# Kernel tuning notes

Hardware: AMD Instinct MI355X
Metric: run time of the kernel (lower is better)

The kernel has to match this reference:

```python
import jax, jax.numpy as jnp
import numpy as np

BETA_MAX = 0.995
BETA_MIN = 0.05
EPI_AGE_PENALTY = 0.02
EPI_STRENGTH_BOOST = 0.5
EPI_STRENGTH_DECAY = 0.995
EPI_WRITE_ALPHA = 0.5
EVICT_AGE_BOOST = 0.05
EVICT_STR_PENALTY = 0.5
SLOT_TEMP = 50.0
SWITCH_TAU = 0.5

B, H, K, U, OBS, SSUM, PROJ = 2048, 256, 32, 128, 128, 128, 128


def setup_inputs() -> dict:
    key = jax.random.key(0)
    ks = jax.random.split(key, 20)
    def gl(k, shape, fan_in):
        return jax.random.normal(k, shape, jnp.float32) / np.sqrt(fan_in).astype(np.float32)
    inp = {}
    inp['h_prev'] = jax.random.normal(ks[0], (B, H), jnp.float32)
    inp['keys'] = jax.random.normal(ks[1], (B, K, H), jnp.float32)
    inp['vals'] = jax.random.normal(ks[2], (B, K, H), jnp.float32)
    inp['age'] = jax.random.uniform(ks[3], (B, K), jnp.float32) * 100.0
    inp['strength'] = jax.random.uniform(ks[4], (B, K), jnp.float32)
    inp['obs'] = jax.random.normal(ks[5], (B, OBS), jnp.float32)
    inp['ssum'] = jax.random.normal(ks[6], (B, SSUM), jnp.float32)
    inp['u_int_prev'] = jax.random.normal(ks[7], (B, U), jnp.float32)
    inp['step_in_macro'] = jax.random.randint(ks[8], (B,), 0, 4, jnp.int32)
    # learned parameters
    inp['W_obs'] = gl(ks[9], (OBS, PROJ), OBS); inp['b_obs'] = jnp.zeros((PROJ,), jnp.float32)
    inp['W_ssum'] = gl(ks[10], (SSUM, PROJ), SSUM); inp['b_ssum'] = jnp.zeros((PROJ,), jnp.float32)
    XIN = 2 * PROJ
    inp['Wi'] = gl(ks[11], (XIN, 3 * H), XIN); inp['bi'] = jnp.zeros((3 * H,), jnp.float32)
    inp['Wh'] = gl(ks[12], (H, 3 * H), H); inp['bhn'] = jnp.zeros((H,), jnp.float32)
    inp['W_gate'] = gl(ks[13], (H, 1), H); inp['b_gate'] = jnp.zeros((1,), jnp.float32)
    inp['W_mean'] = gl(ks[14], (2 * H, U), 2 * H); inp['b_mean'] = jnp.zeros((U,), jnp.float32)
    inp['u_logstd'] = jnp.full((U,), -1.0, jnp.float32)
    inp['W_beta'] = gl(ks[15], (2 * H, 1), 2 * H); inp['b_beta'] = jnp.zeros((1,), jnp.float32)
    inp['W_sw'] = gl(ks[16], (2 * H, 1), 2 * H); inp['b_sw'] = jnp.zeros((1,), jnp.float32)
    return inp


def reference(h_prev, keys, vals, age, strength, obs, ssum, u_int_prev, step_in_macro,
              W_obs, b_obs, W_ssum, b_ssum, Wi, bi, Wh, bhn, W_gate, b_gate,
              W_mean, b_mean, u_logstd, W_beta, b_beta, W_sw, b_sw):
    Kslots = keys.shape[1]
    # input projections + GRU step (flax GRUCell: h' = (1-z)*n + z*h)
    xo = jnp.tanh(obs @ W_obs + b_obs)
    xs = jnp.tanh(ssum @ W_ssum + b_ssum)
    x_in = jnp.concatenate([xo, xs], axis=-1)
    gi = x_in @ Wi + bi
    gh = h_prev @ Wh
    ir, iz, inn = jnp.split(gi, 3, axis=-1)
    hr, hz, hn = jnp.split(gh, 3, axis=-1)
    r = jax.nn.sigmoid(ir + hr)
    z = jax.nn.sigmoid(iz + hz)
    n = jnp.tanh(inn + r * (hn + bhn))
    h_t = (1.0 - z) * n + z * h_prev
    # write gate
    w_str = jax.nn.sigmoid(h_t @ W_gate + b_gate)  # [B,1]
    # episodic slot memory: cosine-sim read
    qn = h_t / (jnp.linalg.norm(h_t, axis=-1, keepdims=True) + 1e-6)
    kn = keys / (jnp.linalg.norm(keys, axis=-1, keepdims=True) + 1e-6)
    sim_r = jnp.einsum('bkd,bd->bk', kn, qn)
    logits = sim_r + EPI_STRENGTH_BOOST * jnp.log(jnp.clip(strength, 1e-3, 1.0)) - EPI_AGE_PENALTY * age
    w_read = jax.nn.softmax(logits, axis=-1)
    read_out = jnp.einsum('bk,bkd->bd', w_read, vals)
    # write addressing (write_vec == query_vec == h_t so sim_w == sim_r)
    wk_n = qn
    sim_w = sim_r
    evict = EVICT_AGE_BOOST * jnp.log1p(age) - EVICT_STR_PENALTY * strength
    write_soft = jax.nn.softmax(sim_w * SLOT_TEMP + evict, axis=-1)
    write_hard = jax.nn.one_hot(jnp.argmax(write_soft, axis=-1), Kslots, dtype=jnp.float32)
    write_w = jax.lax.stop_gradient(write_hard - write_soft) + write_soft  # straight-through
    ws = jnp.clip(w_str, 0.0, 1.0)  # [B,1]
    eff_rate = write_w * ws * EPI_WRITE_ALPHA  # [B,K]
    rate = eff_rate[:, :, None]
    keys_new = (1.0 - rate) * keys + rate * wk_n[:, None, :]
    vals_new = (1.0 - rate) * vals + rate * h_t[:, None, :]
    age_new = (age + 1.0) * (1.0 - write_w)
    str_new = strength * EPI_STRENGTH_DECAY
    str_new = jnp.clip(str_new + write_w * ws * (1.0 - str_new), 0.0, 1.0)
    # heads
    ctx = jnp.concatenate([h_t, read_out], axis=-1)
    mean = ctx @ W_mean + b_mean
    beta = BETA_MIN + (BETA_MAX - BETA_MIN) * jax.nn.sigmoid((ctx @ W_beta + b_beta)[:, 0])
    sw_prob = jax.nn.sigmoid((ctx @ W_sw + b_sw)[:, 0])
    # deterministic path (rng=None): u_prop = mean, threshold switch
    u_prop = mean
    switch_f = jnp.where(sw_prob > SWITCH_TAU, 1.0, 0.0)
    is_boundary = jnp.where(step_in_macro == 0, 1.0, 0.0)
    switch_f = jnp.maximum(switch_f, is_boundary)
    sw_f = switch_f[:, None]
    beta_eff = beta[:, None] * (1.0 - sw_f)
    u_int = beta_eff * u_int_prev + (1.0 - beta_eff) * u_prop
    return (h_t, keys_new, vals_new, age_new, str_new, u_prop,
            switch_f.astype(jnp.int32), u_int, beta, sw_prob)
```

## Files before the change

### kernel.cpp

```cpp
#include <hip/hip_runtime.h>
#include <math.h>

#define Bdim 2048
#define Hdim 256
#define KS 32
#define Udim 128
#define OBSD 128
#define PROJD 128
#define H3 768

__device__ __forceinline__ float sigm(float x){ return 1.0f/(1.0f+__expf(-x)); }

typedef float __attribute__((ext_vector_type(4))) f32x4;

__device__ __forceinline__ float4 ntload4(const float* p){
    f32x4 v = __builtin_nontemporal_load((const f32x4*)p);
    return make_float4(v.x, v.y, v.z, v.w);
}

__global__ __launch_bounds__(256) void kA1(
    const float* __restrict__ obs, const float* __restrict__ ssum,
    const float* __restrict__ W_obs, const float* __restrict__ b_obs,
    const float* __restrict__ W_ssum, const float* __restrict__ b_ssum,
    float* __restrict__ xin)
{
    __shared__ float s_in[2][8][128];
    const int t = threadIdx.x;
    const int r0 = blockIdx.x * 8;

    {
        int r = t >> 5, c4 = (t & 31) << 2;
        float4 v = *(const float4*)(obs + (size_t)(r0+r)*OBSD + c4);
        s_in[0][r][c4+0]=v.x; s_in[0][r][c4+1]=v.y; s_in[0][r][c4+2]=v.z; s_in[0][r][c4+3]=v.w;
        v = *(const float4*)(ssum + (size_t)(r0+r)*OBSD + c4);
        s_in[1][r][c4+0]=v.x; s_in[1][r][c4+1]=v.y; s_in[1][r][c4+2]=v.z; s_in[1][r][c4+3]=v.w;
    }
    __syncthreads();

    const int col = t & 127;
    const int src = t >> 7;
    const float* Wp = src ? W_ssum : W_obs;
    const float bb = src ? b_ssum[col] : b_obs[col];

    float acc[8] = {0,0,0,0,0,0,0,0};
    for (int i=0;i<128;i++){
        float w = Wp[i*PROJD + col];
        #pragma unroll
        for (int r=0;r<8;r++) acc[r] = fmaf(s_in[src][r][i], w, acc[r]);
    }
    #pragma unroll
    for (int r=0;r<8;r++)
        xin[(size_t)(r0+r)*256 + t] = tanhf(acc[r] + bb);
}

__global__ __launch_bounds__(256) void kG2(
    const float* __restrict__ xin, const float* __restrict__ hp,
    const float* __restrict__ Wi, const float* __restrict__ Wh,
    float* __restrict__ g)
{
    __shared__ float Xt[2][16][68];
    __shared__ float Wt[2][16][64];

    const int t = threadIdx.x;
    const int bx = blockIdx.x >> 4;
    const int by = blockIdx.x & 15;
    const int r0 = bx * 64;
    const int c0 = by * 64;

    const int kbeg = (c0 >= 768) ? 256 : 0;
    const int kend = (c0 >= 512 && c0 < 768) ? 256 : 512;
    const int nck  = (kend - kbeg) >> 4;

    const int sr  = t >> 2;
    const int sk4 = (t & 3) << 2;
    const size_t xbase = (size_t)(r0 + sr) * 256 + sk4;
    const int wk  = t >> 4;
    const int wc4 = (t & 15) << 2;
    const int cW  = (c0 < 512) ? c0 : (c0 - 256);

    const int rowA = (t & 15) << 2;
    const int colA = (t >> 4) << 2;

    float acc[4][4] = {{0.f}};
    float4 xr, wr;

    {
        const int k0 = kbeg;
        const float* xs = (k0 < 256) ? (xin + xbase + k0) : (hp + xbase + (k0 - 256));
        xr = *(const float4*)xs;
        const int k = k0 + wk;
        const float* wsrc = (k < 256) ? (Wi + (size_t)k*H3 + c0 + wc4)
                                      : (Wh + (size_t)(k-256)*H3 + cW + wc4);
        wr = *(const float4*)wsrc;
    }
    Xt[0][sk4+0][sr] = xr.x; Xt[0][sk4+1][sr] = xr.y;
    Xt[0][sk4+2][sr] = xr.z; Xt[0][sk4+3][sr] = xr.w;
    *(float4*)&Wt[0][wk][wc4] = wr;
    __syncthreads();

    for (int ck = 0; ck < nck; ck++){
        const int cur = ck & 1;
        const bool more = (ck + 1 < nck);
        if (more){
            const int k0 = kbeg + ((ck + 1) << 4);
            const float* xs = (k0 < 256) ? (xin + xbase + k0) : (hp + xbase + (k0 - 256));
            xr = *(const float4*)xs;
            const int k = k0 + wk;
            const float* wsrc = (k < 256) ? (Wi + (size_t)k*H3 + c0 + wc4)
                                          : (Wh + (size_t)(k-256)*H3 + cW + wc4);
            wr = *(const float4*)wsrc;
        }
        #pragma unroll
        for (int kk = 0; kk < 16; kk++){
            float4 a4 = *(const float4*)&Xt[cur][kk][rowA];
            float4 b4 = *(const float4*)&Wt[cur][kk][colA];
            float av[4] = {a4.x, a4.y, a4.z, a4.w};
            float bv[4] = {b4.x, b4.y, b4.z, b4.w};
            #pragma unroll
            for (int i=0;i<4;i++)
                #pragma unroll
                for (int j=0;j<4;j++)
                    acc[i][j] = fmaf(av[i], bv[j], acc[i][j]);
        }
        if (more){
            const int nxt = cur ^ 1;
            Xt[nxt][sk4+0][sr] = xr.x; Xt[nxt][sk4+1][sr] = xr.y;
            Xt[nxt][sk4+2][sr] = xr.z; Xt[nxt][sk4+3][sr] = xr.w;
            *(float4*)&Wt[nxt][wk][wc4] = wr;
            __syncthreads();
        }
    }

    #pragma unroll
    for (int i=0;i<4;i++){
        float4 o = make_float4(acc[i][0], acc[i][1], acc[i][2], acc[i][3]);
        *(float4*)&g[(size_t)(r0 + rowA + i)*1024 + c0 + colA] = o;
    }
}

__global__ __launch_bounds__(256) void kA3(
    const float* __restrict__ g, const float* __restrict__ h_prev,
    const float* __restrict__ bi, const float* __restrict__ bhn,
    const float* __restrict__ W_gate, const float* __restrict__ b_gate,
    const float* __restrict__ W_beta, const float* __restrict__ W_sw,
    const float* __restrict__ W_mean,
    float* __restrict__ out_h, float* __restrict__ ws_invn, float* __restrict__ ws_wstr,
    float* __restrict__ ws_bh, float* __restrict__ ws_sh, float* __restrict__ ws_meanh)
{
    __shared__ float s_h[4][256];
    __shared__ float redA[4][4], redB[4][4], redC[4][4], redD[4][4];
    const int t = threadIdx.x;
    const int r0 = blockIdx.x * 4;

    const float bir = bi[t], biz = bi[t+256], bin_ = bi[t+512];
    const float bh = bhn[t];
    const float wg = W_gate[t];
    const float wb = W_beta[t];
    const float wsw = W_sw[t];
    const int lane = t & 63, wid = t >> 6;

    float hv[4];
    #pragma unroll
    for (int r=0;r<4;r++){
        const size_t gb = (size_t)(r0+r)*1024;
        float gr = g[gb + t];
        float gz = g[gb + 256 + t];
        float gni = g[gb + 512 + t];
        float gnh = g[gb + 768 + t];
        float hp = h_prev[(size_t)(r0+r)*Hdim + t];
        float rr = sigm(gr + bir);
        float zz = sigm(gz + biz);
        float nn = tanhf(gni + bin_ + rr*(gnh + bh));
        hv[r] = (1.0f - zz)*nn + zz*hp;
        s_h[r][t] = hv[r];
    }

    #pragma unroll
    for (int r=0;r<4;r++){
        float a = hv[r]*hv[r];
        float b2 = hv[r]*wg;
        float c2 = hv[r]*wb;
        float d2 = hv[r]*wsw;
        #pragma unroll
        for (int off=32; off>=1; off>>=1){
            a  += __shfl_down(a, off);
            b2 += __shfl_down(b2, off);
            c2 += __shfl_down(c2, off);
            d2 += __shfl_down(d2, off);
        }
        if (lane==0){ redA[r][wid]=a; redB[r][wid]=b2; redC[r][wid]=c2; redD[r][wid]=d2; }
    }
    __syncthreads();
    if (t < 4){
        float ss = redA[t][0]+redA[t][1]+redA[t][2]+redA[t][3];
        float gd = redB[t][0]+redB[t][1]+redB[t][2]+redB[t][3];
        float cb = redC[t][0]+redC[t][1]+redC[t][2]+redC[t][3];
        float cs = redD[t][0]+redD[t][1]+redD[t][2]+redD[t][3];
        ws_invn[r0+t] = 1.0f/(sqrtf(ss) + 1e-6f);
        ws_wstr[r0+t] = sigm(gd + b_gate[0]);
        ws_bh[r0+t] = cb;
        ws_sh[r0+t] = cs;
    }
    #pragma unroll
    for (int r=0;r<4;r++)
        out_h[(size_t)(r0+r)*Hdim + t] = hv[r];
    __syncthreads();

    {
        const int c4 = (t & 31) << 2;
        const int row = (t >> 6);
        const int kh  = (t >> 5) & 1;
        float acc[4] = {0,0,0,0};
        const float* Wm = W_mean + (size_t)kh*128*Udim + c4;
        const float* hr = s_h[row] + kh*128;
        #pragma unroll 8
        for (int i=0;i<128;i++){
            float4 w4 = *(const float4*)(Wm + (size_t)i*Udim);
            float x = hr[i];
            acc[0] = fmaf(x, w4.x, acc[0]);
            acc[1] = fmaf(x, w4.y, acc[1]);
            acc[2] = fmaf(x, w4.z, acc[2]);
            acc[3] = fmaf(x, w4.w, acc[3]);
        }
        __syncthreads();
        s_h[row][kh*128 + c4 + 0] = acc[0];
        s_h[row][kh*128 + c4 + 1] = acc[1];
        s_h[row][kh*128 + c4 + 2] = acc[2];
        s_h[row][kh*128 + c4 + 3] = acc[3];
        __syncthreads();
        const int row2 = t >> 6;
        const int c2 = (t & 63) << 1;
        #pragma unroll
        for (int j=0;j<2;j++){
            int c = c2 + j;
            ws_meanh[(size_t)(r0+row2)*Udim + c] = s_h[row2][c] + s_h[row2][128 + c];
        }
    }
}

__global__ __launch_bounds__(256) void kBC(
    const float* __restrict__ keys, const float* __restrict__ vals,
    const float* __restrict__ age, const float* __restrict__ strength,
    const float* __restrict__ h_t,
    const float* __restrict__ ws_invn, const float* __restrict__ ws_wstr,
    const float* __restrict__ ws_bh, const float* __restrict__ ws_sh,
    const float* __restrict__ ws_meanh,
    const float* __restrict__ u_int_prev, const int* __restrict__ step_in_macro,
    const float* __restrict__ W_mean, const float* __restrict__ b_mean,
    const float* __restrict__ W_beta, const float* __restrict__ b_beta,
    const float* __restrict__ W_sw, const float* __restrict__ b_sw,
    float* __restrict__ keys_new, float* __restrict__ vals_new,
    float* __restrict__ age_new, float* __restrict__ str_new,
    float* __restrict__ out_uprop, float* __restrict__ out_switch,
    float* __restrict__ out_uint, float* __restrict__ out_beta, float* __restrict__ out_swp)
{
    __shared__ float s_sim[KS], s_wr[KS], s_rate[KS];
    __shared__ float4 s_ro[4][64];
    __shared__ float s_rov[256];
    __shared__ float s_part[2][128];
    __shared__ float s_red[2][4];
    __shared__ float s_beff;

    const int b = blockIdx.x;
    const int t = threadIdx.x, lane = t & 63, wid = t >> 6;

    float ag = 0.f, st = 0.f, wstr = 0.f;
    if (t < KS){
        ag = age[b*KS+t];
        st = strength[b*KS+t];
        wstr = ws_wstr[b];
    }

    const float invn = ws_invn[b];
    const float4 h4 = ((const float4*)(h_t + (size_t)b*Hdim))[lane];
    const float4 q4 = make_float4(h4.x*invn, h4.y*invn, h4.z*invn, h4.w*invn);

    const float* Kb = keys + (size_t)b*KS*Hdim;
    const float* Vb = vals + (size_t)b*KS*Hdim;
    float4 kreg[8], vreg[8];
    float v[16];
    #pragma unroll
    for (int s=0;s<8;s++){
        const int k = wid*8 + s;
        kreg[s] = ntload4(Kb + k*Hdim + lane*4);
        vreg[s] = ntload4(Vb + k*Hdim + lane*4);
        v[2*s]   = kreg[s].x*q4.x + kreg[s].y*q4.y + kreg[s].z*q4.z + kreg[s].w*q4.w;
        v[2*s+1] = kreg[s].x*kreg[s].x + kreg[s].y*kreg[s].y + kreg[s].z*kreg[s].z + kreg[s].w*kreg[s].w;
    }

    {
        const bool hb5 = (lane & 32) != 0;
        #pragma unroll
        for (int i=0;i<8;i++){
            float send = hb5 ? v[i] : v[i+8];
            float recv = __shfl_xor(send, 32);
            v[i] = (hb5 ? v[i+8] : v[i]) + recv;
        }
        const bool hb4 = (lane & 16) != 0;
        #pragma unroll
        for (int i=0;i<4;i++){
            float send = hb4 ? v[i] : v[i+4];
            float recv = __shfl_xor(send, 16);
            v[i] = (hb4 ? v[i+4] : v[i]) + recv;
        }
        const bool hb3 = (lane & 8) != 0;
        #pragma unroll
        for (int i=0;i<2;i++){
            float send = hb3 ? v[i] : v[i+2];
            float recv = __shfl_xor(send, 8);
            v[i] = (hb3 ? v[i+2] : v[i]) + recv;
        }
        const bool hb2 = (lane & 4) != 0;
        {
            float send = hb2 ? v[0] : v[1];
            float recv = __shfl_xor(send, 4);
            v[0] = (hb2 ? v[1] : v[0]) + recv;
        }
        float r0 = v[0];
        r0 += __shfl_xor(r0, 2);
        r0 += __shfl_xor(r0, 1);
        float other = __shfl_xor(r0, 4);
        if ((lane & 7) == 0){
            s_sim[wid*8 + (lane>>3)] = r0 / (sqrtf(other) + 1e-6f);
        }
    }
    __syncthreads();

    if (t < KS){
        float sim = s_sim[t];
        float cl = fminf(fmaxf(st, 0.001f), 1.0f);
        float logit = sim + 0.5f*logf(cl) - 0.02f*ag;
        float wl = 50.0f*sim + 0.05f*log1pf(ag) - 0.5f*st;

        float lmax = logit;
        #pragma unroll
        for (int off=16; off>=1; off>>=1)
            lmax = fmaxf(lmax, __shfl_xor(lmax, off));
        float e = __expf(logit - lmax);
        float es = e;
        #pragma unroll
        for (int off=16; off>=1; off>>=1)
            es += __shfl_xor(es, off);

        float wm = wl; int ki = t;
        #pragma unroll
        for (int off=16; off>=1; off>>=1){
            float ow = __shfl_xor(wm, off);
            int   ok = __shfl_xor(ki, off);
            if (ow > wm || (ow == wm && ok < ki)){ wm = ow; ki = ok; }
        }

        s_wr[t] = e / es;
        float hard = (t == ki) ? 1.0f : 0.0f;
        s_rate[t] = hard * 0.5f * wstr;
        age_new[b*KS+t] = (ag + 1.0f)*(1.0f - hard);
        float sd = st*0.995f;
        float sn = sd + hard*wstr*(1.0f - sd);
        str_new[b*KS+t] = fminf(fmaxf(sn,0.f),1.f);
    }
    __syncthreads();

    float4 ro = make_float4(0.f,0.f,0.f,0.f);
    float* KNb = keys_new + (size_t)b*KS*Hdim;
    float* VNb = vals_new + (size_t)b*KS*Hdim;
    #pragma unroll
    for (int s=0;s<8;s++){
        const int k = wid*8 + s;
        const float wr = s_wr[k];
        const float rate = s_rate[k];
        const float om = 1.0f - rate;
        ro.x = fmaf(wr, vreg[s].x, ro.x);
        ro.y = fmaf(wr, vreg[s].y, ro.y);
        ro.z = fmaf(wr, vreg[s].z, ro.z);
        ro.w = fmaf(wr, vreg[s].w, ro.w);
        float4 kn, vn;
        kn.x = om*kreg[s].x + rate*q4.x;
        kn.y = om*kreg[s].y + rate*q4.y;
        kn.z = om*kreg[s].z + rate*q4.z;
        kn.w = om*kreg[s].w + rate*q4.w;
        vn.x = om*vreg[s].x + rate*h4.x;
        vn.y = om*vreg[s].y + rate*h4.y;
        vn.z = om*vreg[s].z + rate*h4.z;
        vn.w = om*vreg[s].w + rate*h4.w;
        *(float4*)(KNb + k*Hdim + lane*4) = kn;
        *(float4*)(VNb + k*Hdim + lane*4) = vn;
    }
    s_ro[wid][lane] = ro;
    __syncthreads();
    if (t < 64){
        float4 a = s_ro[0][t], bb = s_ro[1][t], c = s_ro[2][t], d = s_ro[3][t];
        s_rov[t*4+0] = a.x+bb.x+c.x+d.x;
        s_rov[t*4+1] = a.y+bb.y+c.y+d.y;
        s_rov[t*4+2] = a.z+bb.z+c.z+d.z;
        s_rov[t*4+3] = a.w+bb.w+c.w+d.w;
    }
    __syncthreads();

    {
        const int col = t & 127;
        const int kh  = t >> 7;
        const float* rop = s_rov + kh*128;
        const float* Wm = W_mean + (size_t)(256 + kh*128)*Udim + col;
        float acc = 0.f;
        #pragma unroll 8
        for (int i=0;i<128;i++)
            acc = fmaf(rop[i], Wm[(size_t)i*Udim], acc);
        s_part[kh][col] = acc;

        float cb = s_rov[t]*W_beta[256+t];
        float cs = s_rov[t]*W_sw[256+t];
        #pragma unroll
        for (int off=32; off>=1; off>>=1){
            cb += __shfl_down(cb, off);
            cs += __shfl_down(cs, off);
        }
        if (lane == 0){ s_red[0][wid] = cb; s_red[1][wid] = cs; }
    }
    __syncthreads();
    if (t == 0){
        float db  = s_red[0][0]+s_red[0][1]+s_red[0][2]+s_red[0][3] + ws_bh[b] + b_beta[0];
        float dsw = s_red[1][0]+s_red[1][1]+s_red[1][2]+s_red[1][3] + ws_sh[b] + b_sw[0];
        float beta = 0.05f + 0.945f*sigm(db);
        float swp = sigm(dsw);
        float swf = (swp > 0.5f) ? 1.0f : 0.0f;
        if (step_in_macro[b] == 0) swf = 1.0f;
        out_beta[b]  = beta;
        out_swp[b]   = swp;
        out_switch[b]= swf;
        s_beff = beta*(1.0f - swf);
    }
    __syncthreads();
    if (t < 128){
        float mean = ws_meanh[(size_t)b*Udim + t] + s_part[0][t] + s_part[1][t] + b_mean[t];
        size_t o = (size_t)b*Udim + t;
        out_uprop[o] = mean;
        float be = s_beff;
        out_uint[o] = be*u_int_prev[o] + (1.0f-be)*mean;
    }
}

extern "C" void kernel_launch(void* const* d_in, const int* in_sizes, int n_in,
                              void* d_out, int out_size, void* d_ws, size_t ws_size,
                              hipStream_t stream)
{
    const float* h_prev   = (const float*)d_in[0];
    const float* keys     = (const float*)d_in[1];
    const float* vals     = (const float*)d_in[2];
    const float* age      = (const float*)d_in[3];
    const float* strength = (const float*)d_in[4];
    const float* obs      = (const float*)d_in[5];
    const float* ssum     = (const float*)d_in[6];
    const float* u_int_prev = (const float*)d_in[7];
    const int*   step     = (const int*)d_in[8];
    const float* W_obs    = (const float*)d_in[9];
    const float* b_obs    = (const float*)d_in[10];
    const float* W_ssum   = (const float*)d_in[11];
    const float* b_ssum   = (const float*)d_in[12];
    const float* Wi       = (const float*)d_in[13];
    const float* bi       = (const float*)d_in[14];
    const float* Wh       = (const float*)d_in[15];
    const float* bhn      = (const float*)d_in[16];
    const float* W_gate   = (const float*)d_in[17];
    const float* b_gate   = (const float*)d_in[18];
    const float* W_mean   = (const float*)d_in[19];
    const float* b_mean   = (const float*)d_in[20];
    const float* W_beta   = (const float*)d_in[22];
    const float* b_beta   = (const float*)d_in[23];
    const float* W_sw     = (const float*)d_in[24];
    const float* b_sw     = (const float*)d_in[25];

    float* out = (float*)d_out;
    float* out_h    = out;
    float* out_kn   = out_h   + 524288;
    float* out_vn   = out_kn  + 16777216;
    float* out_age  = out_vn  + 16777216;
    float* out_str  = out_age + 65536;
    float* out_up   = out_str + 65536;
    float* out_sw   = out_up  + 262144;
    float* out_ui   = out_sw  + 2048;
    float* out_beta = out_ui  + 262144;
    float* out_swp  = out_beta+ 2048;

    float* ws = (float*)d_ws;
    float* ws_invn  = ws;
    float* ws_wstr  = ws + Bdim;
    float* ws_bh    = ws + 2*Bdim;
    float* ws_sh    = ws + 3*Bdim;
    float* ws_meanh = ws + 4*Bdim;

    float* ws_xin = out_vn;
    float* ws_g   = out_kn;

    kA1<<<Bdim/8, 256, 0, stream>>>(obs, ssum, W_obs, b_obs, W_ssum, b_ssum, ws_xin);
    kG2<<<512, 256, 0, stream>>>(ws_xin, h_prev, Wi, Wh, ws_g);
    kA3<<<Bdim/4, 256, 0, stream>>>(ws_g, h_prev, bi, bhn, W_gate, b_gate,
                                    W_beta, W_sw, W_mean,
                                    out_h, ws_invn, ws_wstr, ws_bh, ws_sh, ws_meanh);
    kBC<<<Bdim, 256, 0, stream>>>(keys, vals, age, strength, out_h,
                                  ws_invn, ws_wstr, ws_bh, ws_sh, ws_meanh,
                                  u_int_prev, step, W_mean, b_mean,
                                  W_beta, b_beta, W_sw, b_sw,
                                  out_kn, out_vn, out_age, out_str,
                                  out_up, out_sw, out_ui, out_beta, out_swp);
}
```

Before: 113.7 us.

## Split read-out head projection out of memory kernel into batched kernel

The per-row head matmul (read_out @ W_mean lower half, plus beta/switch dot products) is moved out of the memory-update kernel kBC into a new kernel kC2 that processes four rows per block. kBC now only writes the reduced read vector to workspace. This lets each W_mean load be reused across several rows instead of re-reading the whole weight slice per batch row, and shortens the memory-bound kBC tail. It costs an extra launch and a small workspace round trip.

```diff
diff --git a/kernel.cpp b/kernel.cpp
--- a/kernel.cpp
+++ b/kernel.cpp
@@ -243,23 +243,12 @@
     const float* __restrict__ age, const float* __restrict__ strength,
     const float* __restrict__ h_t,
     const float* __restrict__ ws_invn, const float* __restrict__ ws_wstr,
-    const float* __restrict__ ws_bh, const float* __restrict__ ws_sh,
-    const float* __restrict__ ws_meanh,
-    const float* __restrict__ u_int_prev, const int* __restrict__ step_in_macro,
-    const float* __restrict__ W_mean, const float* __restrict__ b_mean,
-    const float* __restrict__ W_beta, const float* __restrict__ b_beta,
-    const float* __restrict__ W_sw, const float* __restrict__ b_sw,
     float* __restrict__ keys_new, float* __restrict__ vals_new,
     float* __restrict__ age_new, float* __restrict__ str_new,
-    float* __restrict__ out_uprop, float* __restrict__ out_switch,
-    float* __restrict__ out_uint, float* __restrict__ out_beta, float* __restrict__ out_swp)
+    float* __restrict__ ws_ro)
 {
     __shared__ float s_sim[KS], s_wr[KS], s_rate[KS];
     __shared__ float4 s_ro[4][64];
-    __shared__ float s_rov[256];
-    __shared__ float s_part[2][128];
-    __shared__ float s_red[2][4];
-    __shared__ float s_beff;
 
     const int b = blockIdx.x;
     const int t = threadIdx.x, lane = t & 63, wid = t >> 6;
@@ -389,52 +378,84 @@
     __syncthreads();
     if (t < 64){
         float4 a = s_ro[0][t], bb = s_ro[1][t], c = s_ro[2][t], d = s_ro[3][t];
-        s_rov[t*4+0] = a.x+bb.x+c.x+d.x;
-        s_rov[t*4+1] = a.y+bb.y+c.y+d.y;
-        s_rov[t*4+2] = a.z+bb.z+c.z+d.z;
-        s_rov[t*4+3] = a.w+bb.w+c.w+d.w;
-    }
-    __syncthreads();
+        float4 r;
+        r.x = a.x+bb.x+c.x+d.x;
+        r.y = a.y+bb.y+c.y+d.y;
+        r.z = a.z+bb.z+c.z+d.z;
+        r.w = a.w+bb.w+c.w+d.w;
+        ((float4*)(ws_ro + (size_t)b*Hdim))[t] = r;
+    }
+}
+
+__global__ __launch_bounds__(256) void kC2(
+    const float* __restrict__ ws_ro, const float* __restrict__ ws_meanh,
+    const float* __restrict__ ws_bh, const float* __restrict__ ws_sh,
+    const float* __restrict__ u_int_prev, const int* __restrict__ step_in_macro,
+    const float* __restrict__ W_mean, const float* __restrict__ b_mean,
+    const float* __restrict__ W_beta, const float* __restrict__ b_beta,
+    const float* __restrict__ W_sw, const float* __restrict__ b_sw,
+    float* __restrict__ out_uprop, float* __restrict__ out_switch,
+    float* __restrict__ out_uint, float* __restrict__ out_beta, float* __restrict__ out_swp)
+{
+    __shared__ float s_ro[4][256];
+    __shared__ float redb[4][4], reds[4][4];
+    __shared__ float s_beff[4];
+    const int t = threadIdx.x;
+    const int r0 = blockIdx.x * 4;
 
     {
-        const int col = t & 127;
-        const int kh  = t >> 7;
-        const float* rop = s_rov + kh*128;
-        const float* Wm = W_mean + (size_t)(256 + kh*128)*Udim + col;
-        float acc = 0.f;
-        #pragma unroll 8
-        for (int i=0;i<128;i++)
-            acc = fmaf(rop[i], Wm[(size_t)i*Udim], acc);
-        s_part[kh][col] = acc;
-
-        float cb = s_rov[t]*W_beta[256+t];
-        float cs = s_rov[t]*W_sw[256+t];
-        #pragma unroll
-        for (int off=32; off>=1; off>>=1){
-            cb += __shfl_down(cb, off);
-            cs += __shfl_down(cs, off);
-        }
-        if (lane == 0){ s_red[0][wid] = cb; s_red[1][wid] = cs; }
-    }
-    __syncthreads();
-    if (t == 0){
-        float db  = s_red[0][0]+s_red[0][1]+s_red[0][2]+s_red[0][3] + ws_bh[b] + b_beta[0];
-        float dsw = s_red[1][0]+s_red[1][1]+s_red[1][2]+s_red[1][3] + ws_sh[b] + b_sw[0];
+        int r = t >> 6, c4 = (t & 63) << 2;
+        float4 v = *(const float4*)(ws_ro + (size_t)(r0+r)*Hdim + c4);
+        s_ro[r][c4+0]=v.x; s_ro[r][c4+1]=v.y; s_ro[r][c4+2]=v.z; s_ro[r][c4+3]=v.w;
+    }
+    __syncthreads();
+
+    const int col = t & 127;
+    const int rh = t >> 7;
+    float acc[2] = {0.f, 0.f};
+    #pragma unroll 8
+    for (int i=0;i<256;i++){
+        float w = W_mean[(size_t)(256+i)*Udim + col];
+        acc[0] = fmaf(s_ro[2*rh+0][i], w, acc[0]);
+        acc[1] = fmaf(s_ro[2*rh+1][i], w, acc[1]);
+    }
+
+    {
+        const float wb = W_beta[256+t], wsw = W_sw[256+t];
+        const int lane = t & 63, wid = t >> 6;
+        #pragma unroll
+        for (int r=0;r<4;r++){
+            float cb = s_ro[r][t]*wb;
+            float cs = s_ro[r][t]*wsw;
+            #pragma unroll
+            for (int off=32; off>=1; off>>=1){
+                cb += __shfl_down(cb, off);
+                cs += __shfl_down(cs, off);
+            }
+            if (lane==0){ redb[r][wid]=cb; reds[r][wid]=cs; }
+        }
+    }
+    __syncthreads();
+    if (t < 4){
+        float db  = redb[t][0]+redb[t][1]+redb[t][2]+redb[t][3] + ws_bh[r0+t] + b_beta[0];
+        float dsw = reds[t][0]+reds[t][1]+reds[t][2]+reds[t][3] + ws_sh[r0+t] + b_sw[0];
         float beta = 0.05f + 0.945f*sigm(db);
         float swp = sigm(dsw);
         float swf = (swp > 0.5f) ? 1.0f : 0.0f;
-        if (step_in_macro[b] == 0) swf = 1.0f;
-        out_beta[b]  = beta;
-        out_swp[b]   = swp;
-        out_switch[b]= swf;
-        s_beff = beta*(1.0f - swf);
-    }
-    __syncthreads();
-    if (t < 128){
-        float mean = ws_meanh[(size_t)b*Udim + t] + s_part[0][t] + s_part[1][t] + b_mean[t];
-        size_t o = (size_t)b*Udim + t;
+        if (step_in_macro[r0+t] == 0) swf = 1.0f;
+        out_beta[r0+t] = beta;
+        out_swp[r0+t] = swp;
+        out_switch[r0+t] = swf;
+        s_beff[t] = beta*(1.0f - swf);
+    }
+    __syncthreads();
+    #pragma unroll
+    for (int j=0;j<2;j++){
+        int r = 2*rh + j;
+        float mean = ws_meanh[(size_t)(r0+r)*Udim + col] + acc[j] + b_mean[col];
+        size_t o = (size_t)(r0+r)*Udim + col;
         out_uprop[o] = mean;
-        float be = s_beff;
+        float be = s_beff[r];
         out_uint[o] = be*u_int_prev[o] + (1.0f-be)*mean;
     }
 }
@@ -487,6 +508,7 @@
     float* ws_bh    = ws + 2*Bdim;
     float* ws_sh    = ws + 3*Bdim;
     float* ws_meanh = ws + 4*Bdim;
+    float* ws_ro    = ws + 4*Bdim + Bdim*Udim;
 
     float* ws_xin = out_vn;
     float* ws_g   = out_kn;
@@ -497,9 +519,10 @@
                                     W_beta, W_sw, W_mean,
                                     out_h, ws_invn, ws_wstr, ws_bh, ws_sh, ws_meanh);
     kBC<<<Bdim, 256, 0, stream>>>(keys, vals, age, strength, out_h,
-                                  ws_invn, ws_wstr, ws_bh, ws_sh, ws_meanh,
-                                  u_int_prev, step, W_mean, b_mean,
-                                  W_beta, b_beta, W_sw, b_sw,
-                                  out_kn, out_vn, out_age, out_str,
-                                  out_up, out_sw, out_ui, out_beta, out_swp);
-}
+                                  ws_invn, ws_wstr,
+                                  out_kn, out_vn, out_age, out_str, ws_ro);
+    kC2<<<Bdim/4, 256, 0, stream>>>(ws_ro, ws_meanh, ws_bh, ws_sh,
+                                    u_int_prev, step, W_mean, b_mean,
+                                    W_beta, b_beta, W_sw, b_sw,
+                                    out_up, out_sw, out_ui, out_beta, out_swp);
+}
```

New measurement: 120.5 us. +6.0%, slower.
